# Kernel optimization log

Measured on AMD Instinct MI355X. Metric: run time of the kernel, lower is better.

Reference implementation:

```python
import jax, jax.numpy as jnp
import numpy as np

# fp4 e2m1 positive value grid and midpoints between adjacent grid values
_GRID = jnp.array([0.0, 0.5, 1.0, 1.5, 2.0, 3.0, 4.0, 6.0], dtype=jnp.float32)
_MIDS = jnp.array([0.25, 0.75, 1.25, 1.75, 2.5, 3.5, 5.0], dtype=jnp.float32)
BLOCK = 32               # MX block size
E8M0_BIAS = 127
F32_MIN_NORMAL = float(2.0 ** -126)
F4_E2M1_MAX_POW2 = 2     # log2 of largest power-of-two <= 6.0 -> 4.0


def _quantize_fp4(a):
    """Round-to-nearest-even onto the signed e2m1 grid."""
    mag = jnp.clip(jnp.abs(a), 0.0, 6.0)
    idx = jnp.searchsorted(_MIDS, mag, side='left')  # ties round down
    mids_pad = jnp.concatenate([_MIDS, jnp.array([-1.0], jnp.float32)])
    tie = mag == mids_pad[idx]
    idx = jnp.where(tie & (idx % 2 == 1), idx + 1, idx)  # ties-to-even mantissa
    return _GRID[idx] * jnp.where(a < 0, -1.0, 1.0)


def _floor_log2(m):
    """Exact floor(log2(m)) for m > 0, with corrections for fp rounding of log2."""
    e = jnp.floor(jnp.log2(m))
    e = jnp.where(jnp.exp2(e) > m, e - 1.0, e)
    e = jnp.where(jnp.exp2(e + 1.0) <= m, e + 1.0, e)
    return e


def _qdq_mxfp4(x):
    """Quantize-dequantize x to MX fp4_e2m1, block 32, FLOOR scale mode (to_mx + to_dtype)."""
    shp = x.shape
    xb = x.reshape(-1, BLOCK)
    max_abs = jnp.max(jnp.abs(xb), axis=1)
    eps = F32_MIN_NORMAL * (max_abs == 0).astype(jnp.float32)
    pow2 = _floor_log2(max_abs + eps)
    e_unb = jnp.clip(pow2 - F4_E2M1_MAX_POW2, -float(E8M0_BIAS), float(E8M0_BIAS) + 1.0)
    scale = jnp.maximum(jnp.exp2(e_unb), F32_MIN_NORMAL)  # [nblk]
    q = _quantize_fp4(xb / scale[:, None])
    return (q * scale[:, None]).reshape(shp)


def _dequant_weight(weight_packed, weight_scale, out_f, in_f):
    """Unpack uint8-packed fp4 (low nibble first), apply e8m0 block scales."""
    p = weight_packed.astype(jnp.int32)
    low = p & 0xF
    high = (p >> 4) & 0xF
    nib = jnp.stack([low, high], axis=-1).reshape(out_f, in_f)  # interleave low,high
    vals = _GRID[nib & 7] * jnp.where((nib & 8) > 0, -1.0, 1.0)
    s = jnp.exp2(weight_scale.astype(jnp.float32) - E8M0_BIAS)  # get_fp_scale(e8m0)
    return (vals.reshape(-1, BLOCK) * s[:, None]).reshape(out_f, in_f)


def setup_inputs() -> dict:
    key = jax.random.key(0)
    k1, k2, k3 = jax.random.split(key, 3)
    M, IN, OUT = 4096, 4096, 4096
    x = jax.random.normal(k1, (M, IN), dtype=jnp.float32)
    weight_packed = jax.random.randint(k2, (OUT, IN // 2), 0, 256, dtype=jnp.int32)
    weight_scale = jax.random.randint(k3, (OUT * IN // BLOCK,), 0, 135, dtype=jnp.int32)
    return {"x": x, "weight_packed": weight_packed, "weight_scale": weight_scale}


def reference(x, weight_packed, weight_scale):
    out_f = weight_packed.shape[0]
    in_f = weight_packed.shape[1] * 2
    xq = _qdq_mxfp4(x)                                       # qdq_mxfp4(x)
    w_dq = _dequant_weight(weight_packed, weight_scale, out_f, in_f)
    return xq @ w_dq.T                                       # matmul(x, w_dq.t())
```

## Files before the change

kernel.cpp:

```cpp
#include <hip/hip_runtime.h>
#include <stdint.h>

typedef __attribute__((ext_vector_type(4)))  int   intx4;
typedef __attribute__((ext_vector_type(8)))  int   intx8;
typedef __attribute__((ext_vector_type(16))) float floatx16;

#define GLL16(gp, lp)                                                               \
    __builtin_amdgcn_global_load_lds((const __attribute__((address_space(1))) unsigned int*)(gp), \
                                     (__attribute__((address_space(3))) unsigned int*)(lp), 16, 0, 0)
#define GLL4(gp, lp)                                                                \
    __builtin_amdgcn_global_load_lds((const __attribute__((address_space(1))) unsigned int*)(gp), \
                                     (__attribute__((address_space(3))) unsigned int*)(lp), 4, 0, 0)

__device__ __forceinline__ uint32_t enc1(float xv, float inv) {
    float a = fminf(fabsf(xv) * inv, 6.0f);
    int e;
    if (a < 2.0f)      e = (int)rintf(a + a);
    else if (a < 4.0f) e = (int)rintf(a) + 2;
    else               e = (int)rintf(a * 0.5f) + 4;
    return (uint32_t)e | ((__float_as_uint(xv) >> 28) & 8u);
}

__global__ __launch_bounds__(256) void quant_x_kernel(const float* __restrict__ x,
                                                      uint32_t* __restrict__ xq,
                                                      uint8_t* __restrict__ xs_t,
                                                      int M, int K) {
    int t = blockIdx.x * 256 + threadIdx.x;
    int kbpr = K >> 5;
    int m = t / kbpr;
    int kb = t - m * kbpr;
    const float4* src = (const float4*)(x + (size_t)m * K + (size_t)kb * 32);
    float4 v[8];
#pragma unroll
    for (int i = 0; i < 8; ++i) v[i] = src[i];
    float mx = 0.f;
#pragma unroll
    for (int i = 0; i < 8; ++i)
        mx = fmaxf(mx, fmaxf(fmaxf(fabsf(v[i].x), fabsf(v[i].y)),
                             fmaxf(fabsf(v[i].z), fabsf(v[i].w))));
    unsigned ef = __float_as_uint(mx) >> 23;
    unsigned code = (ef < 3u) ? 1u : (ef - 2u);
    float inv = __uint_as_float((254u - code) << 23);

    uint32_t w[4];
#pragma unroll
    for (int d = 0; d < 4; ++d) {
        float4 va = v[2 * d], vb = v[2 * d + 1];
        w[d] =  enc1(va.x, inv)        | (enc1(va.y, inv) << 4)
             | (enc1(va.z, inv) << 8)  | (enc1(va.w, inv) << 12)
             | (enc1(vb.x, inv) << 16) | (enc1(vb.y, inv) << 20)
             | (enc1(vb.z, inv) << 24) | (enc1(vb.w, inv) << 28);
    }
    ((uint4*)xq)[t] = make_uint4(w[0], w[1], w[2], w[3]);
    xs_t[(size_t)kb * M + m] = (uint8_t)code;
}

__global__ __launch_bounds__(256) void tscale_kernel(const int* __restrict__ wsc,
                                                     uint8_t* __restrict__ ws_t,
                                                     int N, int kbpr) {
    int t = blockIdx.x * 256 + threadIdx.x;
    int n = t / kbpr;
    int kb = t - n * kbpr;
    ws_t[(size_t)kb * N + n] = (uint8_t)wsc[t];
}

__global__ __launch_bounds__(256) void repack_w_kernel(const int* __restrict__ wp,
                                                       uint32_t* __restrict__ wrep,
                                                       int n4) {
    int t = blockIdx.x * 256 + threadIdx.x;
    if (t >= n4) return;
    int4 p = ((const int4*)wp)[t];
    wrep[t] = (uint32_t)(p.x & 0xFF) | ((uint32_t)(p.y & 0xFF) << 8)
            | ((uint32_t)(p.z & 0xFF) << 16) | ((uint32_t)(p.w & 0xFF) << 24);
}

__global__ __launch_bounds__(256) void gemm_mx_kernel(const uint8_t* __restrict__ Apk,
                                                      const uint8_t* __restrict__ Bpk,
                                                      const uint8_t* __restrict__ AsT,
                                                      const uint8_t* __restrict__ BsT,
                                                      float* __restrict__ C,
                                                      int M, int N, int K) {
    __shared__ __align__(16) uint8_t sA[8192];
    __shared__ __align__(16) uint8_t sB[8192];
    __shared__ __align__(16) uint8_t sAs[512];
    __shared__ __align__(16) uint8_t sBs[512];

    const int tid = threadIdx.x;
    const int bm0 = blockIdx.y << 7;
    const int bn0 = blockIdx.x << 7;
    const int wave = tid >> 6;
    const int lane = tid & 63;
    const int wm = (wave >> 1) << 6;
    const int wn = (wave & 1) << 6;
    const int row = lane & 31;
    const int h = lane >> 5;
    const int Kb = K >> 1;

    const int s0 = tid, s1 = tid + 256;
    const int r0 = s0 >> 2, p0 = (s0 & 3) ^ (r0 & 3);
    const int r1 = s1 >> 2, p1 = (s1 & 3) ^ (r1 & 3);
    const uint8_t* Ag0 = Apk + (size_t)(bm0 + r0) * Kb + p0 * 16;
    const uint8_t* Ag1 = Apk + (size_t)(bm0 + r1) * Kb + p1 * 16;
    const uint8_t* Bg0 = Bpk + (size_t)(bn0 + r0) * Kb + p0 * 16;
    const uint8_t* Bg1 = Bpk + (size_t)(bn0 + r1) * Kb + p1 * 16;

    const int st = tid & 127;
    const int sj = st >> 5, si = st & 31;
    const uint8_t* Sg = (tid < 128) ? (AsT + (size_t)sj * M + bm0 + si * 4)
                                    : (BsT + (size_t)sj * N + bn0 + si * 4);
    uint8_t* Sl = (tid < 128) ? (sAs + st * 4) : (sBs + st * 4);
    const size_t sAdv = (size_t)4 * (size_t)((tid < 128) ? M : N);

    floatx16 acc[2][2];
#pragma unroll
    for (int a = 0; a < 2; ++a)
#pragma unroll
        for (int b = 0; b < 2; ++b)
#pragma unroll
            for (int r = 0; r < 16; ++r) acc[a][b][r] = 0.f;

    const int nchunk = K >> 7;
    for (int c = 0; c < nchunk; ++c) {
        __syncthreads();
        const size_t koff = (size_t)c << 6;
        GLL16(Ag0 + koff, sA + s0 * 16);
        GLL16(Ag1 + koff, sA + s1 * 16);
        GLL16(Bg0 + koff, sB + s0 * 16);
        GLL16(Bg1 + koff, sB + s1 * 16);
        GLL4(Sg + (size_t)c * sAdv, Sl);
        __syncthreads();

#pragma unroll
        for (int s = 0; s < 2; ++s) {
            intx4 a4[2], b4[2];
            int sa[2], sb[2];
            const int kp = 2 * s + h;
#pragma unroll
            for (int mt = 0; mt < 2; ++mt) {
                const int lr = wm + mt * 32 + row;
                a4[mt] = *(const intx4*)(sA + lr * 64 + ((kp ^ (lr & 3)) << 4));
                sa[mt] = sAs[kp * 128 + lr];
            }
#pragma unroll
            for (int nt = 0; nt < 2; ++nt) {
                const int lr = wn + nt * 32 + row;
                b4[nt] = *(const intx4*)(sB + lr * 64 + ((kp ^ (lr & 3)) << 4));
                sb[nt] = sBs[kp * 128 + lr];
            }
#pragma unroll
            for (int mt = 0; mt < 2; ++mt)
#pragma unroll
                for (int nt = 0; nt < 2; ++nt) {
                    intx8 a8 = {a4[mt][0], a4[mt][1], a4[mt][2], a4[mt][3], 0, 0, 0, 0};
                    intx8 b8 = {b4[nt][0], b4[nt][1], b4[nt][2], b4[nt][3], 0, 0, 0, 0};
                    acc[mt][nt] = __builtin_amdgcn_mfma_scale_f32_32x32x64_f8f6f4(
                        a8, b8, acc[mt][nt], 4, 4, 0, sa[mt], 0, sb[nt]);
                }
        }
    }

#pragma unroll
    for (int mt = 0; mt < 2; ++mt)
#pragma unroll
        for (int nt = 0; nt < 2; ++nt) {
            const int col = bn0 + wn + nt * 32 + row;
#pragma unroll
            for (int g = 0; g < 4; ++g) {
                const int rw = bm0 + wm + mt * 32 + 8 * g + 4 * h;
#pragma unroll
                for (int q = 0; q < 4; ++q)
                    C[(size_t)(rw + q) * N + col] = acc[mt][nt][4 * g + q];
            }
        }
}

extern "C" void kernel_launch(void* const* d_in, const int* in_sizes, int n_in,
                              void* d_out, int out_size, void* d_ws, size_t ws_size,
                              hipStream_t stream) {
    const float* x = (const float*)d_in[0];
    const int* wp = (const int*)d_in[1];
    const int* wsc = (const int*)d_in[2];
    float* out = (float*)d_out;

    const int K = 4096;
    const int M = in_sizes[0] / K;
    const int N = (in_sizes[1] * 2) / K;
    const int kbpr = K / 32;
    const int npack = N * K / 2;

    uint32_t* xq   = (uint32_t*)d_ws;
    uint8_t*  xs   = (uint8_t*)d_ws + (size_t)M * K / 2;
    uint8_t*  wst  = xs + (size_t)M * kbpr;
    uint32_t* wrep = (uint32_t*)(wst + (size_t)N * kbpr);

    quant_x_kernel<<<(M * kbpr) / 256, 256, 0, stream>>>(x, xq, xs, M, K);
    tscale_kernel<<<(N * kbpr) / 256, 256, 0, stream>>>(wsc, wst, N, kbpr);
    repack_w_kernel<<<(npack / 4 + 255) / 256, 256, 0, stream>>>(wp, wrep, npack / 4);

    dim3 grid(N / 128, M / 128);
    gemm_mx_kernel<<<grid, 256, 0, stream>>>((const uint8_t*)xq, (const uint8_t*)wrep,
                                             xs, wst, out, M, N, K);
}
```

Measured before the change: 204.0 us.

## Enlarge GEMM tile to 256x256, double-buffer LDS, restructure quantize and scale layouts

The GEMM block tile grows from 128x128 to 256x256, with a 4x4 MFMA subtile per wave and launch bounds of 256 threads and one block. LDS staging becomes double-buffered so the next K chunk is prefetched while the current one is computed, and the swizzle changes. The x-quantize kernel now handles 8 elements per thread, combining block maxima with warp shuffles, and writes scales row-major instead of transposed. Weight-scale transposition is replaced by a byte pack fused into the weight repack kernel. The larger tile cuts global traffic per FLOP, but only 256 blocks are launched and register pressure from 16 accumulators is high.

```diff
diff --git a/kernel.cpp b/kernel.cpp
--- a/kernel.cpp
+++ b/kernel.cpp
@@ -23,134 +23,136 @@
 
 __global__ __launch_bounds__(256) void quant_x_kernel(const float* __restrict__ x,
                                                       uint32_t* __restrict__ xq,
-                                                      uint8_t* __restrict__ xs_t,
-                                                      int M, int K) {
+                                                      uint8_t* __restrict__ xs) {
     int t = blockIdx.x * 256 + threadIdx.x;
-    int kbpr = K >> 5;
-    int m = t / kbpr;
-    int kb = t - m * kbpr;
-    const float4* src = (const float4*)(x + (size_t)m * K + (size_t)kb * 32);
-    float4 v[8];
-#pragma unroll
-    for (int i = 0; i < 8; ++i) v[i] = src[i];
-    float mx = 0.f;
-#pragma unroll
-    for (int i = 0; i < 8; ++i)
-        mx = fmaxf(mx, fmaxf(fmaxf(fabsf(v[i].x), fabsf(v[i].y)),
-                             fmaxf(fabsf(v[i].z), fabsf(v[i].w))));
+    const float4* src = (const float4*)(x + (size_t)t * 8);
+    float4 v0 = src[0], v1 = src[1];
+    float mx = fmaxf(fmaxf(fmaxf(fabsf(v0.x), fabsf(v0.y)), fmaxf(fabsf(v0.z), fabsf(v0.w))),
+                     fmaxf(fmaxf(fabsf(v1.x), fabsf(v1.y)), fmaxf(fabsf(v1.z), fabsf(v1.w))));
+    mx = fmaxf(mx, __shfl_xor(mx, 1, 64));
+    mx = fmaxf(mx, __shfl_xor(mx, 2, 64));
     unsigned ef = __float_as_uint(mx) >> 23;
     unsigned code = (ef < 3u) ? 1u : (ef - 2u);
     float inv = __uint_as_float((254u - code) << 23);
 
-    uint32_t w[4];
-#pragma unroll
-    for (int d = 0; d < 4; ++d) {
-        float4 va = v[2 * d], vb = v[2 * d + 1];
-        w[d] =  enc1(va.x, inv)        | (enc1(va.y, inv) << 4)
-             | (enc1(va.z, inv) << 8)  | (enc1(va.w, inv) << 12)
-             | (enc1(vb.x, inv) << 16) | (enc1(vb.y, inv) << 20)
-             | (enc1(vb.z, inv) << 24) | (enc1(vb.w, inv) << 28);
-    }
-    ((uint4*)xq)[t] = make_uint4(w[0], w[1], w[2], w[3]);
-    xs_t[(size_t)kb * M + m] = (uint8_t)code;
-}
-
-__global__ __launch_bounds__(256) void tscale_kernel(const int* __restrict__ wsc,
-                                                     uint8_t* __restrict__ ws_t,
-                                                     int N, int kbpr) {
+    uint32_t w =  enc1(v0.x, inv)        | (enc1(v0.y, inv) << 4)
+               | (enc1(v0.z, inv) << 8)  | (enc1(v0.w, inv) << 12)
+               | (enc1(v1.x, inv) << 16) | (enc1(v1.y, inv) << 20)
+               | (enc1(v1.z, inv) << 24) | (enc1(v1.w, inv) << 28);
+    xq[t] = w;
+    if ((threadIdx.x & 3) == 0) xs[t >> 2] = (uint8_t)code;
+}
+
+__global__ __launch_bounds__(256) void repack_kernel(const int* __restrict__ wp,
+                                                     const int* __restrict__ wsc,
+                                                     uint32_t* __restrict__ wrep,
+                                                     uint32_t* __restrict__ wscb,
+                                                     int n4w, int n4s) {
     int t = blockIdx.x * 256 + threadIdx.x;
-    int n = t / kbpr;
-    int kb = t - n * kbpr;
-    ws_t[(size_t)kb * N + n] = (uint8_t)wsc[t];
-}
-
-__global__ __launch_bounds__(256) void repack_w_kernel(const int* __restrict__ wp,
-                                                       uint32_t* __restrict__ wrep,
-                                                       int n4) {
-    int t = blockIdx.x * 256 + threadIdx.x;
-    if (t >= n4) return;
-    int4 p = ((const int4*)wp)[t];
-    wrep[t] = (uint32_t)(p.x & 0xFF) | ((uint32_t)(p.y & 0xFF) << 8)
-            | ((uint32_t)(p.z & 0xFF) << 16) | ((uint32_t)(p.w & 0xFF) << 24);
-}
-
-__global__ __launch_bounds__(256) void gemm_mx_kernel(const uint8_t* __restrict__ Apk,
-                                                      const uint8_t* __restrict__ Bpk,
-                                                      const uint8_t* __restrict__ AsT,
-                                                      const uint8_t* __restrict__ BsT,
-                                                      float* __restrict__ C,
-                                                      int M, int N, int K) {
-    __shared__ __align__(16) uint8_t sA[8192];
-    __shared__ __align__(16) uint8_t sB[8192];
-    __shared__ __align__(16) uint8_t sAs[512];
-    __shared__ __align__(16) uint8_t sBs[512];
+    if (t < n4w) {
+        int4 p = ((const int4*)wp)[t];
+        wrep[t] = (uint32_t)(p.x & 0xFF) | ((uint32_t)(p.y & 0xFF) << 8)
+                | ((uint32_t)(p.z & 0xFF) << 16) | ((uint32_t)(p.w & 0xFF) << 24);
+    } else if (t - n4w < n4s) {
+        int u = t - n4w;
+        int4 p = ((const int4*)wsc)[u];
+        wscb[u] = (uint32_t)(p.x & 0xFF) | ((uint32_t)(p.y & 0xFF) << 8)
+                | ((uint32_t)(p.z & 0xFF) << 16) | ((uint32_t)(p.w & 0xFF) << 24);
+    }
+}
+
+__global__ __launch_bounds__(256, 1) void gemm_mx_kernel(const uint8_t* __restrict__ Apk,
+                                                         const uint8_t* __restrict__ Bpk,
+                                                         const uint8_t* __restrict__ As,
+                                                         const uint8_t* __restrict__ Bs,
+                                                         float* __restrict__ C,
+                                                         int M, int N, int K) {
+    __shared__ __align__(16) uint8_t sA[2][16384];
+    __shared__ __align__(16) uint8_t sB[2][16384];
+    __shared__ __align__(16) uint8_t sAs[2][1024];
+    __shared__ __align__(16) uint8_t sBs[2][1024];
 
     const int tid = threadIdx.x;
-    const int bm0 = blockIdx.y << 7;
-    const int bn0 = blockIdx.x << 7;
+    const int bm0 = blockIdx.y << 8;
+    const int bn0 = blockIdx.x << 8;
     const int wave = tid >> 6;
     const int lane = tid & 63;
-    const int wm = (wave >> 1) << 6;
-    const int wn = (wave & 1) << 6;
+    const int wm = (wave >> 1) << 7;
+    const int wn = (wave & 1) << 7;
     const int row = lane & 31;
     const int h = lane >> 5;
     const int Kb = K >> 1;
-
-    const int s0 = tid, s1 = tid + 256;
-    const int r0 = s0 >> 2, p0 = (s0 & 3) ^ (r0 & 3);
-    const int r1 = s1 >> 2, p1 = (s1 & 3) ^ (r1 & 3);
-    const uint8_t* Ag0 = Apk + (size_t)(bm0 + r0) * Kb + p0 * 16;
-    const uint8_t* Ag1 = Apk + (size_t)(bm0 + r1) * Kb + p1 * 16;
-    const uint8_t* Bg0 = Bpk + (size_t)(bn0 + r0) * Kb + p0 * 16;
-    const uint8_t* Bg1 = Bpk + (size_t)(bn0 + r1) * Kb + p1 * 16;
-
-    const int st = tid & 127;
-    const int sj = st >> 5, si = st & 31;
-    const uint8_t* Sg = (tid < 128) ? (AsT + (size_t)sj * M + bm0 + si * 4)
-                                    : (BsT + (size_t)sj * N + bn0 + si * 4);
-    uint8_t* Sl = (tid < 128) ? (sAs + st * 4) : (sBs + st * 4);
-    const size_t sAdv = (size_t)4 * (size_t)((tid < 128) ? M : N);
-
-    floatx16 acc[2][2];
-#pragma unroll
-    for (int a = 0; a < 2; ++a)
-#pragma unroll
-        for (int b = 0; b < 2; ++b)
+    const int kbpr = K >> 5;
+
+    int soff[4];
+    const uint8_t* Aga[4];
+    const uint8_t* Bga[4];
+#pragma unroll
+    for (int i = 0; i < 4; ++i) {
+        int s = tid + 256 * i;
+        int r = s >> 2;
+        int p = (s & 3) ^ ((r >> 1) & 3);
+        soff[i] = s * 16;
+        Aga[i] = Apk + (size_t)(bm0 + r) * Kb + p * 16;
+        Bga[i] = Bpk + (size_t)(bn0 + r) * Kb + p * 16;
+    }
+    const uint8_t* Asg = As + (size_t)(bm0 + tid) * kbpr;
+    const uint8_t* Bsg = Bs + (size_t)(bn0 + tid) * kbpr;
+
+    floatx16 acc[4][4];
+#pragma unroll
+    for (int a = 0; a < 4; ++a)
+#pragma unroll
+        for (int b = 0; b < 4; ++b)
 #pragma unroll
             for (int r = 0; r < 16; ++r) acc[a][b][r] = 0.f;
 
     const int nchunk = K >> 7;
+
+#pragma unroll
+    for (int i = 0; i < 4; ++i) {
+        GLL16(Aga[i], sA[0] + soff[i]);
+        GLL16(Bga[i], sB[0] + soff[i]);
+    }
+    GLL4(Asg, sAs[0] + tid * 4);
+    GLL4(Bsg, sBs[0] + tid * 4);
+
     for (int c = 0; c < nchunk; ++c) {
+        const int buf = c & 1;
         __syncthreads();
-        const size_t koff = (size_t)c << 6;
-        GLL16(Ag0 + koff, sA + s0 * 16);
-        GLL16(Ag1 + koff, sA + s1 * 16);
-        GLL16(Bg0 + koff, sB + s0 * 16);
-        GLL16(Bg1 + koff, sB + s1 * 16);
-        GLL4(Sg + (size_t)c * sAdv, Sl);
-        __syncthreads();
+        if (c + 1 < nchunk) {
+            const int nb = buf ^ 1;
+            const size_t koff = (size_t)(c + 1) * 64;
+#pragma unroll
+            for (int i = 0; i < 4; ++i) {
+                GLL16(Aga[i] + koff, sA[nb] + soff[i]);
+                GLL16(Bga[i] + koff, sB[nb] + soff[i]);
+            }
+            GLL4(Asg + (c + 1) * 4, sAs[nb] + tid * 4);
+            GLL4(Bsg + (c + 1) * 4, sBs[nb] + tid * 4);
+        }
 
 #pragma unroll
         for (int s = 0; s < 2; ++s) {
-            intx4 a4[2], b4[2];
-            int sa[2], sb[2];
             const int kp = 2 * s + h;
-#pragma unroll
-            for (int mt = 0; mt < 2; ++mt) {
+            intx4 a4[4], b4[4];
+            int sa[4], sb[4];
+#pragma unroll
+            for (int mt = 0; mt < 4; ++mt) {
                 const int lr = wm + mt * 32 + row;
-                a4[mt] = *(const intx4*)(sA + lr * 64 + ((kp ^ (lr & 3)) << 4));
-                sa[mt] = sAs[kp * 128 + lr];
-            }
-#pragma unroll
-            for (int nt = 0; nt < 2; ++nt) {
+                a4[mt] = *(const intx4*)(sA[buf] + (lr * 4 + (kp ^ ((lr >> 1) & 3))) * 16);
+                sa[mt] = sAs[buf][lr * 4 + kp];
+            }
+#pragma unroll
+            for (int nt = 0; nt < 4; ++nt) {
                 const int lr = wn + nt * 32 + row;
-                b4[nt] = *(const intx4*)(sB + lr * 64 + ((kp ^ (lr & 3)) << 4));
-                sb[nt] = sBs[kp * 128 + lr];
-            }
-#pragma unroll
-            for (int mt = 0; mt < 2; ++mt)
-#pragma unroll
-                for (int nt = 0; nt < 2; ++nt) {
+                b4[nt] = *(const intx4*)(sB[buf] + (lr * 4 + (kp ^ ((lr >> 1) & 3))) * 16);
+                sb[nt] = sBs[buf][lr * 4 + kp];
+            }
+#pragma unroll
+            for (int mt = 0; mt < 4; ++mt)
+#pragma unroll
+                for (int nt = 0; nt < 4; ++nt) {
                     intx8 a8 = {a4[mt][0], a4[mt][1], a4[mt][2], a4[mt][3], 0, 0, 0, 0};
                     intx8 b8 = {b4[nt][0], b4[nt][1], b4[nt][2], b4[nt][3], 0, 0, 0, 0};
                     acc[mt][nt] = __builtin_amdgcn_mfma_scale_f32_32x32x64_f8f6f4(
@@ -160,9 +162,9 @@
     }
 
 #pragma unroll
-    for (int mt = 0; mt < 2; ++mt)
-#pragma unroll
-        for (int nt = 0; nt < 2; ++nt) {
+    for (int mt = 0; mt < 4; ++mt)
+#pragma unroll
+        for (int nt = 0; nt < 4; ++nt) {
             const int col = bn0 + wn + nt * 32 + row;
 #pragma unroll
             for (int g = 0; g < 4; ++g) {
@@ -187,17 +189,20 @@
     const int N = (in_sizes[1] * 2) / K;
     const int kbpr = K / 32;
     const int npack = N * K / 2;
+    const int nsc = N * kbpr;
 
     uint32_t* xq   = (uint32_t*)d_ws;
     uint8_t*  xs   = (uint8_t*)d_ws + (size_t)M * K / 2;
-    uint8_t*  wst  = xs + (size_t)M * kbpr;
-    uint32_t* wrep = (uint32_t*)(wst + (size_t)N * kbpr);
-
-    quant_x_kernel<<<(M * kbpr) / 256, 256, 0, stream>>>(x, xq, xs, M, K);
-    tscale_kernel<<<(N * kbpr) / 256, 256, 0, stream>>>(wsc, wst, N, kbpr);
-    repack_w_kernel<<<(npack / 4 + 255) / 256, 256, 0, stream>>>(wp, wrep, npack / 4);
-
-    dim3 grid(N / 128, M / 128);
+    uint32_t* wrep = (uint32_t*)(xs + (size_t)M * kbpr);
+    uint8_t*  wscb = (uint8_t*)wrep + (size_t)npack;
+
+    quant_x_kernel<<<(M * K / 8) / 256, 256, 0, stream>>>(x, xq, xs);
+
+    int n4w = npack / 4, n4s = nsc / 4;
+    repack_kernel<<<(n4w + n4s + 255) / 256, 256, 0, stream>>>(wp, wsc, wrep,
+                                                               (uint32_t*)wscb, n4w, n4s);
+
+    dim3 grid(N / 256, M / 256);
     gemm_mx_kernel<<<grid, 256, 0, stream>>>((const uint8_t*)xq, (const uint8_t*)wrep,
-                                             xs, wst, out, M, N, K);
-}
+                                             xs, wscb, out, M, N, K);
+}
```

After: 208.7 us. 2.3% more time.
